# Kernel tuning notes

Measured on AMD Instinct MI355X. Metric: run time of the kernel, lower is better.

## Reference

```python
import jax, jax.numpy as jnp
import numpy as np

NUM_EXPERTS = 8
HIDDEN = 1024
FFN = 2048
TOKENS = 2048


def setup_inputs() -> dict:
    key = jax.random.key(0)
    k_x, k_idx, k_w1, k_w2 = jax.random.split(key, 4)
    scale = 0.02
    x = jax.random.normal(k_x, (TOKENS, HIDDEN), dtype=jnp.float32)
    expert_indices = jax.random.randint(k_idx, (TOKENS,), 0, NUM_EXPERTS, dtype=jnp.int64)
    W1 = jax.random.normal(k_w1, (NUM_EXPERTS, HIDDEN, FFN), dtype=jnp.float32) * scale
    b1 = jnp.zeros((NUM_EXPERTS, FFN), dtype=jnp.float32)
    W2 = jax.random.normal(k_w2, (NUM_EXPERTS, FFN, HIDDEN), dtype=jnp.float32) * scale
    b2 = jnp.zeros((NUM_EXPERTS, HIDDEN), dtype=jnp.float32)
    return {"x": x, "expert_indices": expert_indices, "W1": W1, "b1": b1, "W2": W2, "b2": b2}


def reference(x, expert_indices, W1, b1, W2, b2):
    # Each token routed to one expert's MLP: Linear -> GELU(exact) -> Linear.
    # Dropout is identity in eval mode. Loop is over the small fixed expert set.
    out = jnp.zeros_like(x)
    for e in range(NUM_EXPERTS):
        h = jax.nn.gelu(x @ W1[e] + b1[e], approximate=False)  # [T, FFN]
        y = h @ W2[e] + b2[e]                                   # [T, H]
        mask = (expert_indices == e)[:, None]
        out = out + jnp.where(mask, y, 0.0)
    return out
```

## Files before the change

kernel.cpp:

```cpp
#include <hip/hip_runtime.h>

#define T_TOK 2048
#define HID   1024
#define FFN   2048
#define NEXP  8
#define MAX_SLOTS 40

typedef __attribute__((ext_vector_type(8))) short bf16x8;
typedef __attribute__((ext_vector_type(4))) float f32x4;

__device__ __forceinline__ short f2bf(float f) {
    unsigned u = __builtin_bit_cast(unsigned, f);
    u = (u + 0x7fffu + ((u >> 16) & 1u)) >> 16;
    return (short)u;
}

__device__ __forceinline__ float gelu_exact(float x) {
    return 0.5f * x * (1.0f + erff(x * 0.70710678118654752f));
}

__device__ __forceinline__ void async_cp16(const short* g, short* l) {
    __builtin_amdgcn_global_load_lds(
        (const __attribute__((address_space(1))) unsigned int*)g,
        (__attribute__((address_space(3))) unsigned int*)l, 16, 0, 0);
}

__device__ __forceinline__ void wtrans_body(
        const float* __restrict__ W, short* __restrict__ WT,
        int K, int N, int e, int kblk, int nblk) {
    int tid = threadIdx.x;
    int w = tid >> 6, l = tid & 63;
    int kb = kblk * 32 + w * 8;
    int n4 = nblk * 256 + l * 4;
    const float* src = W + (size_t)e * K * N + (size_t)kb * N + n4;
    float4 v[8];
#pragma unroll
    for (int r = 0; r < 8; r++)
        v[r] = *(const float4*)(src + (size_t)r * N);
    int kpanel = kb >> 6;
    int kc = (kb >> 3) & 7;
    int npanel = n4 >> 7;
    int n_in = n4 & 127;
    int kpanels = K >> 6;
    short* dst = WT + (size_t)e * K * N
               + ((size_t)npanel * kpanels + kpanel) * 8192
               + kc * 1024 + n_in * 8;
#pragma unroll
    for (int j = 0; j < 4; j++) {
        bf16x8 o = {f2bf(((const float*)&v[0])[j]), f2bf(((const float*)&v[1])[j]),
                    f2bf(((const float*)&v[2])[j]), f2bf(((const float*)&v[3])[j]),
                    f2bf(((const float*)&v[4])[j]), f2bf(((const float*)&v[5])[j]),
                    f2bf(((const float*)&v[6])[j]), f2bf(((const float*)&v[7])[j])};
        *(bf16x8*)(dst + j * 8) = o;
    }
}

__global__ __launch_bounds__(256) void prep_kernel(
        const float* __restrict__ x, const int* __restrict__ idx,
        const float* __restrict__ b2,
        const float* __restrict__ W1, const float* __restrict__ W2,
        short* __restrict__ xb, float* __restrict__ out,
        short* __restrict__ W1T, short* __restrict__ W2T,
        int* __restrict__ offs, int* __restrict__ cnts,
        int* __restrict__ tokl,
        int* __restrict__ slot_e, int* __restrict__ slot_t0) {
    int bx = blockIdx.x;
    int tid = threadIdx.x;
    if (bx < 2048) {
        int e = bx >> 8, rem = bx & 255;
        wtrans_body(W1, W1T, HID, FFN, e, rem & 31, rem >> 5);
    } else if (bx < 4096) {
        int b = bx - 2048;
        int e = b >> 8, rem = b & 255;
        wtrans_body(W2, W2T, FFN, HID, e, rem & 63, rem >> 6);
    } else if (bx < 5120) {
        int i = ((bx - 4096) * 256 + tid) * 8;
        float4 v0 = *(const float4*)(x + i);
        float4 v1 = *(const float4*)(x + i + 4);
        bf16x8 r = {f2bf(v0.x), f2bf(v0.y), f2bf(v0.z), f2bf(v0.w),
                    f2bf(v1.x), f2bf(v1.y), f2bf(v1.z), f2bf(v1.w)};
        *(bf16x8*)(xb + i) = r;
    } else if (bx < 7168) {
        int t = bx - 5120;
        int e = idx[t];
        ((float4*)(out + (size_t)t * HID))[tid] =
            ((const float4*)(b2 + (size_t)e * HID))[tid];
    } else {
        __shared__ int c[NEXP], cur[NEXP], o[NEXP];
        if (tid < NEXP) { c[tid] = 0; cur[tid] = 0; }
        __syncthreads();
        for (int t = tid; t < T_TOK; t += 256) atomicAdd(&c[idx[t]], 1);
        __syncthreads();
        if (tid == 0) {
            int s = 0;
            for (int e = 0; e < NEXP; e++) { o[e] = s; s += c[e]; }
            int ns = 0;
            for (int e = 0; e < NEXP; e++)
                for (int t0 = 0; t0 < c[e]; t0 += 64) {
                    slot_e[ns] = e; slot_t0[ns] = t0; ns++;
                }
            for (; ns < MAX_SLOTS; ns++) slot_e[ns] = -1;
        }
        __syncthreads();
        if (tid < NEXP) { offs[tid] = o[tid]; cnts[tid] = c[tid]; }
        for (int t = tid; t < T_TOK; t += 256) {
            int e = idx[t];
            int p = o[e] + atomicAdd(&cur[e], 1);
            tokl[p] = t;
        }
    }
}

__global__ __launch_bounds__(256) void gemm1_kernel(
        const short* __restrict__ xb, const short* __restrict__ W1T,
        const float* __restrict__ b1,
        const int* __restrict__ offs, const int* __restrict__ cnts,
        const int* __restrict__ tokl,
        const int* __restrict__ slot_e, const int* __restrict__ slot_t0,
        short* __restrict__ hg) {
    int s = blockIdx.y;
    int e = slot_e[s];
    if (e < 0) return;
    int t0 = slot_t0[s], count = cnts[e], off = offs[e];
    int n0 = blockIdx.x * 128;

    __shared__ short As[64 * 64];
    __shared__ short Bs[8 * 128 * 8];
    __shared__ int stok[64];

    int tid = threadIdx.x;
    if (tid < 64) {
        int p = t0 + tid;
        stok[tid] = tokl[off + (p < count ? p : count - 1)];
    }
    __syncthreads();

    int w = tid >> 6, l = tid & 63, l15 = l & 15, quad = l >> 4;
    int wm = (w >> 1) * 32, wn = (w & 1) * 64;

    int m0 = w * 16 + (l >> 3), m1 = m0 + 8;
    int cs = l & 7;
    int c0 = (cs - m0) & 7, c1 = (cs - m1) & 7;
    const short* gA0 = xb + (size_t)stok[m0] * HID + c0 * 8;
    const short* gA1 = xb + (size_t)stok[m1] * HID + c1 * 8;
    short* lA0 = As + w * 1024 + l * 8;
    short* lA1 = lA0 + 512;

    const short* Bpan = W1T + (size_t)e * (FFN * HID)
                      + (size_t)(n0 >> 7) * ((HID >> 6) * 8192);
    int bo0 = (2 * w) * 1024 + l * 8;
    int bo1 = bo0 + 1024;
    int bo2 = bo0 + 512;
    int bo3 = bo1 + 512;

    f32x4 acc[2][4];
#pragma unroll
    for (int i = 0; i < 2; i++)
#pragma unroll
        for (int j = 0; j < 4; j++) acc[i][j] = (f32x4){0.f, 0.f, 0.f, 0.f};

    for (int kt = 0; kt < HID / 64; kt++) {
        const short* bp = Bpan + kt * 8192;
        async_cp16(gA0, lA0);
        async_cp16(gA1, lA1);
        async_cp16(bp + bo0, Bs + bo0);
        async_cp16(bp + bo1, Bs + bo1);
        async_cp16(bp + bo2, Bs + bo2);
        async_cp16(bp + bo3, Bs + bo3);
        gA0 += 64; gA1 += 64;
        __syncthreads();
        bf16x8 a[2][2], b[2][4];
#pragma unroll
        for (int kk = 0; kk < 2; kk++) {
#pragma unroll
            for (int mt = 0; mt < 2; mt++) {
                int m = wm + mt * 16 + l15;
                a[kk][mt] = *(const bf16x8*)&As[m * 64 + (((kk * 4 + quad) + m) & 7) * 8];
            }
#pragma unroll
            for (int nt = 0; nt < 4; nt++) {
                int n = wn + nt * 16 + l15;
                b[kk][nt] = *(const bf16x8*)&Bs[(kk * 4 + quad) * 1024 + n * 8];
            }
        }
#pragma unroll
        for (int kk = 0; kk < 2; kk++)
#pragma unroll
            for (int mt = 0; mt < 2; mt++)
#pragma unroll
                for (int nt = 0; nt < 4; nt++)
                    acc[mt][nt] = __builtin_amdgcn_mfma_f32_16x16x32_bf16(
                        a[kk][mt], b[kk][nt], acc[mt][nt], 0, 0, 0);
        __syncthreads();
    }

    const float* b1e = b1 + e * FFN + n0;
#pragma unroll
    for (int mt = 0; mt < 2; mt++) {
        int rbase = wm + mt * 16 + quad * 4;
#pragma unroll
        for (int nt = 0; nt < 4; nt++) {
            int coln = wn + nt * 16 + l15;
            float bb = b1e[coln];
#pragma unroll
            for (int r = 0; r < 4; r++) {
                int p = t0 + rbase + r;
                if (p < count)
                    hg[(size_t)(off + p) * FFN + n0 + coln] =
                        f2bf(gelu_exact(acc[mt][nt][r] + bb));
            }
        }
    }
}

__global__ __launch_bounds__(256) void gemm2_kernel(
        const short* __restrict__ hg, const short* __restrict__ W2T,
        const int* __restrict__ offs, const int* __restrict__ cnts,
        const int* __restrict__ tokl,
        const int* __restrict__ slot_e, const int* __restrict__ slot_t0,
        float* __restrict__ out) {
    int s = blockIdx.y;
    int e = slot_e[s];
    if (e < 0) return;
    int t0 = slot_t0[s], count = cnts[e], off = offs[e];
    int ks = blockIdx.z;
    int n0 = blockIdx.x * 128;

    __shared__ short As[64 * 64];
    __shared__ short Bs[8 * 128 * 8];

    int tid = threadIdx.x;
    int w = tid >> 6, l = tid & 63, l15 = l & 15, quad = l >> 4;
    int wm = (w >> 1) * 32, wn = (w & 1) * 64;

    int m0 = w * 16 + (l >> 3), m1 = m0 + 8;
    int cs = l & 7;
    int c0 = (cs - m0) & 7, c1 = (cs - m1) & 7;
    int g0 = off + (t0 + m0 < count ? t0 + m0 : count - 1);
    int g1 = off + (t0 + m1 < count ? t0 + m1 : count - 1);
    const short* gA0 = hg + (size_t)g0 * FFN + ks * 1024 + c0 * 8;
    const short* gA1 = hg + (size_t)g1 * FFN + ks * 1024 + c1 * 8;
    short* lA0 = As + w * 1024 + l * 8;
    short* lA1 = lA0 + 512;

    const short* Bpan = W2T + (size_t)e * (FFN * HID)
                      + (size_t)(n0 >> 7) * ((FFN >> 6) * 8192)
                      + (size_t)ks * 16 * 8192;
    int bo0 = (2 * w) * 1024 + l * 8;
    int bo1 = bo0 + 1024;
    int bo2 = bo0 + 512;
    int bo3 = bo1 + 512;

    f32x4 acc[2][4];
#pragma unroll
    for (int i = 0; i < 2; i++)
#pragma unroll
        for (int j = 0; j < 4; j++) acc[i][j] = (f32x4){0.f, 0.f, 0.f, 0.f};

    for (int kt = 0; kt < 16; kt++) {
        const short* bp = Bpan + kt * 8192;
        async_cp16(gA0, lA0);
        async_cp16(gA1, lA1);
        async_cp16(bp + bo0, Bs + bo0);
        async_cp16(bp + bo1, Bs + bo1);
        async_cp16(bp + bo2, Bs + bo2);
        async_cp16(bp + bo3, Bs + bo3);
        gA0 += 64; gA1 += 64;
        __syncthreads();
        bf16x8 a[2][2], b[2][4];
#pragma unroll
        for (int kk = 0; kk < 2; kk++) {
#pragma unroll
            for (int mt = 0; mt < 2; mt++) {
                int m = wm + mt * 16 + l15;
                a[kk][mt] = *(const bf16x8*)&As[m * 64 + (((kk * 4 + quad) + m) & 7) * 8];
            }
#pragma unroll
            for (int nt = 0; nt < 4; nt++) {
                int n = wn + nt * 16 + l15;
                b[kk][nt] = *(const bf16x8*)&Bs[(kk * 4 + quad) * 1024 + n * 8];
            }
        }
#pragma unroll
        for (int kk = 0; kk < 2; kk++)
#pragma unroll
            for (int mt = 0; mt < 2; mt++)
#pragma unroll
                for (int nt = 0; nt < 4; nt++)
                    acc[mt][nt] = __builtin_amdgcn_mfma_f32_16x16x32_bf16(
                        a[kk][mt], b[kk][nt], acc[mt][nt], 0, 0, 0);
        __syncthreads();
    }

#pragma unroll
    for (int mt = 0; mt < 2; mt++) {
        int rbase = wm + mt * 16 + quad * 4;
#pragma unroll
        for (int nt = 0; nt < 4; nt++) {
            int coln = n0 + wn + nt * 16 + l15;
#pragma unroll
            for (int r = 0; r < 4; r++) {
                int p = t0 + rbase + r;
                if (p < count) {
                    int tok = tokl[off + p];
                    atomicAdd(out + (size_t)tok * HID + coln, acc[mt][nt][r]);
                }
            }
        }
    }
}

extern "C" void kernel_launch(void* const* d_in, const int* in_sizes, int n_in,
                              void* d_out, int out_size, void* d_ws, size_t ws_size,
                              hipStream_t stream) {
    const float* x   = (const float*)d_in[0];
    const int*   idx = (const int*)d_in[1];
    const float* W1  = (const float*)d_in[2];
    const float* b1  = (const float*)d_in[3];
    const float* W2  = (const float*)d_in[4];
    const float* b2  = (const float*)d_in[5];
    float* out = (float*)d_out;

    const size_t META = 32768;
    int*   offs    = (int*)d_ws;
    int*   cnts    = offs + 8;
    int*   tokl    = offs + 16;
    int*   slot_e  = offs + 16 + T_TOK;
    int*   slot_t0 = slot_e + MAX_SLOTS;
    char*  base    = (char*)d_ws + META;
    short* xb  = (short*)base;
    short* hg  = (short*)(base + (size_t)T_TOK * HID * 2);
    short* W1T = (short*)(base + (size_t)T_TOK * HID * 2 + (size_t)T_TOK * FFN * 2);
    short* W2T = W1T + (size_t)NEXP * FFN * HID;

    prep_kernel<<<7169, 256, 0, stream>>>(
        x, idx, b2, W1, W2, xb, out, W1T, W2T,
        offs, cnts, tokl, slot_e, slot_t0);

    gemm1_kernel<<<dim3(FFN / 128, MAX_SLOTS), 256, 0, stream>>>(
        xb, W1T, b1, offs, cnts, tokl, slot_e, slot_t0, hg);
    gemm2_kernel<<<dim3(HID / 128, MAX_SLOTS, 2), 256, 0, stream>>>(
        hg, W2T, offs, cnts, tokl, slot_e, slot_t0, out);
}
```

Baseline: 224.6 us.

## Enlarge GEMM M-tile to 128, double-buffer LDS, and swizzle weight panels

Both expert GEMMs move from 64x128 to 128x128 block tiles with 4x4 MFMA accumulators per wave, and routing slots now cover 128 tokens, with MAX_SLOTS cut to 32. The K loop uses two LDS buffers: the async global-to-LDS copy for the next K tile is issued right after the barrier, so it overlaps the MFMAs on the current tile. The weight pre-transpose writes an n-major, XOR-style swizzled panel layout matching the new B-fragment reads, and each prep block now converts two K-chunks. The aim is more reuse per loaded tile, hidden load latency and fewer prep blocks. The cost is higher register and LDS use per block, which may lower occupancy, and more padded rows for experts whose token counts do not fill a 128-row tile.

```diff
diff --git a/kernel.cpp b/kernel.cpp
--- a/kernel.cpp
+++ b/kernel.cpp
@@ -4,7 +4,7 @@
 #define HID   1024
 #define FFN   2048
 #define NEXP  8
-#define MAX_SLOTS 40
+#define MAX_SLOTS 32
 
 typedef __attribute__((ext_vector_type(8))) short bf16x8;
 typedef __attribute__((ext_vector_type(4))) float f32x4;
@@ -27,31 +27,30 @@
 
 __device__ __forceinline__ void wtrans_body(
         const float* __restrict__ W, short* __restrict__ WT,
-        int K, int N, int e, int kblk, int nblk) {
+        int K, int N, int e, int kpanel, int npair) {
     int tid = threadIdx.x;
     int w = tid >> 6, l = tid & 63;
-    int kb = kblk * 32 + w * 8;
-    int n4 = nblk * 256 + l * 4;
-    const float* src = W + (size_t)e * K * N + (size_t)kb * N + n4;
-    float4 v[8];
-#pragma unroll
-    for (int r = 0; r < 8; r++)
-        v[r] = *(const float4*)(src + (size_t)r * N);
-    int kpanel = kb >> 6;
-    int kc = (kb >> 3) & 7;
-    int npanel = n4 >> 7;
-    int n_in = n4 & 127;
-    int kpanels = K >> 6;
-    short* dst = WT + (size_t)e * K * N
-               + ((size_t)npanel * kpanels + kpanel) * 8192
-               + kc * 1024 + n_in * 8;
-#pragma unroll
-    for (int j = 0; j < 4; j++) {
-        bf16x8 o = {f2bf(((const float*)&v[0])[j]), f2bf(((const float*)&v[1])[j]),
-                    f2bf(((const float*)&v[2])[j]), f2bf(((const float*)&v[3])[j]),
-                    f2bf(((const float*)&v[4])[j]), f2bf(((const float*)&v[5])[j]),
-                    f2bf(((const float*)&v[6])[j]), f2bf(((const float*)&v[7])[j])};
-        *(bf16x8*)(dst + j * 8) = o;
+    int n4 = npair * 256 + l * 4;
+    int npanel = n4 >> 7, n_in = n4 & 127;
+    short* dstp = WT + (size_t)e * K * N
+                + ((size_t)npanel * (K >> 6) + kpanel) * 8192;
+    const float* We = W + (size_t)e * K * N;
+#pragma unroll
+    for (int h = 0; h < 2; h++) {
+        int kc = w + h * 4;
+        const float* src = We + (size_t)(kpanel * 64 + kc * 8) * N + n4;
+        float4 v[8];
+#pragma unroll
+        for (int r = 0; r < 8; r++) v[r] = *(const float4*)(src + (size_t)r * N);
+#pragma unroll
+        for (int j = 0; j < 4; j++) {
+            bf16x8 o = {f2bf(((const float*)&v[0])[j]), f2bf(((const float*)&v[1])[j]),
+                        f2bf(((const float*)&v[2])[j]), f2bf(((const float*)&v[3])[j]),
+                        f2bf(((const float*)&v[4])[j]), f2bf(((const float*)&v[5])[j]),
+                        f2bf(((const float*)&v[6])[j]), f2bf(((const float*)&v[7])[j])};
+            int n = n_in + j;
+            *(bf16x8*)(dstp + n * 64 + ((kc + n) & 7) * 8) = o;
+        }
     }
 }
 
@@ -66,22 +65,22 @@
         int* __restrict__ slot_e, int* __restrict__ slot_t0) {
     int bx = blockIdx.x;
     int tid = threadIdx.x;
-    if (bx < 2048) {
-        int e = bx >> 8, rem = bx & 255;
-        wtrans_body(W1, W1T, HID, FFN, e, rem & 31, rem >> 5);
-    } else if (bx < 4096) {
-        int b = bx - 2048;
-        int e = b >> 8, rem = b & 255;
-        wtrans_body(W2, W2T, FFN, HID, e, rem & 63, rem >> 6);
-    } else if (bx < 5120) {
-        int i = ((bx - 4096) * 256 + tid) * 8;
+    if (bx < 1024) {
+        int e = bx >> 7, rem = bx & 127;
+        wtrans_body(W1, W1T, HID, FFN, e, rem >> 3, rem & 7);
+    } else if (bx < 2048) {
+        int b = bx - 1024;
+        int e = b >> 7, rem = b & 127;
+        wtrans_body(W2, W2T, FFN, HID, e, rem >> 2, rem & 3);
+    } else if (bx < 3072) {
+        int i = ((bx - 2048) * 256 + tid) * 8;
         float4 v0 = *(const float4*)(x + i);
         float4 v1 = *(const float4*)(x + i + 4);
         bf16x8 r = {f2bf(v0.x), f2bf(v0.y), f2bf(v0.z), f2bf(v0.w),
                     f2bf(v1.x), f2bf(v1.y), f2bf(v1.z), f2bf(v1.w)};
         *(bf16x8*)(xb + i) = r;
-    } else if (bx < 7168) {
-        int t = bx - 5120;
+    } else if (bx < 5120) {
+        int t = bx - 3072;
         int e = idx[t];
         ((float4*)(out + (size_t)t * HID))[tid] =
             ((const float4*)(b2 + (size_t)e * HID))[tid];
@@ -96,7 +95,7 @@
             for (int e = 0; e < NEXP; e++) { o[e] = s; s += c[e]; }
             int ns = 0;
             for (int e = 0; e < NEXP; e++)
-                for (int t0 = 0; t0 < c[e]; t0 += 64) {
+                for (int t0 = 0; t0 < c[e]; t0 += 128) {
                     slot_e[ns] = e; slot_t0[ns] = t0; ns++;
                 }
             for (; ns < MAX_SLOTS; ns++) slot_e[ns] = -1;
@@ -124,79 +123,74 @@
     int t0 = slot_t0[s], count = cnts[e], off = offs[e];
     int n0 = blockIdx.x * 128;
 
-    __shared__ short As[64 * 64];
-    __shared__ short Bs[8 * 128 * 8];
-    __shared__ int stok[64];
+    __shared__ short As[2][128 * 64];
+    __shared__ short Bs[2][128 * 64];
 
     int tid = threadIdx.x;
-    if (tid < 64) {
-        int p = t0 + tid;
-        stok[tid] = tokl[off + (p < count ? p : count - 1)];
-    }
-    __syncthreads();
-
     int w = tid >> 6, l = tid & 63, l15 = l & 15, quad = l >> 4;
-    int wm = (w >> 1) * 32, wn = (w & 1) * 64;
-
-    int m0 = w * 16 + (l >> 3), m1 = m0 + 8;
-    int cs = l & 7;
-    int c0 = (cs - m0) & 7, c1 = (cs - m1) & 7;
-    const short* gA0 = xb + (size_t)stok[m0] * HID + c0 * 8;
-    const short* gA1 = xb + (size_t)stok[m1] * HID + c1 * 8;
-    short* lA0 = As + w * 1024 + l * 8;
-    short* lA1 = lA0 + 512;
+    int wm = (w >> 1) * 64, wn = (w & 1) * 64;
+
+    const short* srcA[4];
+    int arow[4];
+#pragma unroll
+    for (int i = 0; i < 4; i++) {
+        int row = w * 32 + i * 8 + (l >> 3);
+        arow[i] = row;
+        int c = ((l & 7) - row) & 7;
+        int p = t0 + row;
+        int g = tokl[off + (p < count ? p : count - 1)];
+        srcA[i] = xb + (size_t)g * HID + c * 8;
+    }
+    int sbase = w * 2048 + l * 8;
 
     const short* Bpan = W1T + (size_t)e * (FFN * HID)
                       + (size_t)(n0 >> 7) * ((HID >> 6) * 8192);
-    int bo0 = (2 * w) * 1024 + l * 8;
-    int bo1 = bo0 + 1024;
-    int bo2 = bo0 + 512;
-    int bo3 = bo1 + 512;
-
-    f32x4 acc[2][4];
-#pragma unroll
-    for (int i = 0; i < 2; i++)
+
+    f32x4 acc[4][4];
+#pragma unroll
+    for (int i = 0; i < 4; i++)
 #pragma unroll
         for (int j = 0; j < 4; j++) acc[i][j] = (f32x4){0.f, 0.f, 0.f, 0.f};
 
-    for (int kt = 0; kt < HID / 64; kt++) {
-        const short* bp = Bpan + kt * 8192;
-        async_cp16(gA0, lA0);
-        async_cp16(gA1, lA1);
-        async_cp16(bp + bo0, Bs + bo0);
-        async_cp16(bp + bo1, Bs + bo1);
-        async_cp16(bp + bo2, Bs + bo2);
-        async_cp16(bp + bo3, Bs + bo3);
-        gA0 += 64; gA1 += 64;
-        __syncthreads();
-        bf16x8 a[2][2], b[2][4];
+#define G1_DMA(BUF, KT) {                                                    \
+    _Pragma("unroll") for (int i = 0; i < 4; i++)                            \
+        async_cp16(srcA[i] + (KT) * 64, &As[BUF][sbase + i * 512]);          \
+    const short* bp = Bpan + (size_t)(KT) * 8192;                            \
+    _Pragma("unroll") for (int i = 0; i < 4; i++)                            \
+        async_cp16(bp + sbase + i * 512, &Bs[BUF][sbase + i * 512]); }
+
+    G1_DMA(0, 0);
+    const int NK = HID / 64;
+    for (int kt = 0; kt < NK; kt++) {
+        __syncthreads();
+        int cur = kt & 1;
+        if (kt + 1 < NK) G1_DMA(1 - cur, kt + 1);
 #pragma unroll
         for (int kk = 0; kk < 2; kk++) {
-#pragma unroll
-            for (int mt = 0; mt < 2; mt++) {
+            int cq = kk * 4 + quad;
+            bf16x8 a[4], b[4];
+#pragma unroll
+            for (int mt = 0; mt < 4; mt++) {
                 int m = wm + mt * 16 + l15;
-                a[kk][mt] = *(const bf16x8*)&As[m * 64 + (((kk * 4 + quad) + m) & 7) * 8];
+                a[mt] = *(const bf16x8*)&As[cur][m * 64 + ((cq + m) & 7) * 8];
             }
 #pragma unroll
             for (int nt = 0; nt < 4; nt++) {
                 int n = wn + nt * 16 + l15;
-                b[kk][nt] = *(const bf16x8*)&Bs[(kk * 4 + quad) * 1024 + n * 8];
-            }
-        }
-#pragma unroll
-        for (int kk = 0; kk < 2; kk++)
-#pragma unroll
-            for (int mt = 0; mt < 2; mt++)
+                b[nt] = *(const bf16x8*)&Bs[cur][n * 64 + ((cq + n) & 7) * 8];
+            }
+#pragma unroll
+            for (int mt = 0; mt < 4; mt++)
 #pragma unroll
                 for (int nt = 0; nt < 4; nt++)
                     acc[mt][nt] = __builtin_amdgcn_mfma_f32_16x16x32_bf16(
-                        a[kk][mt], b[kk][nt], acc[mt][nt], 0, 0, 0);
-        __syncthreads();
+                        a[mt], b[nt], acc[mt][nt], 0, 0, 0);
+        }
     }
 
     const float* b1e = b1 + e * FFN + n0;
 #pragma unroll
-    for (int mt = 0; mt < 2; mt++) {
+    for (int mt = 0; mt < 4; mt++) {
         int rbase = wm + mt * 16 + quad * 4;
 #pragma unroll
         for (int nt = 0; nt < 4; nt++) {
@@ -226,74 +220,72 @@
     int ks = blockIdx.z;
     int n0 = blockIdx.x * 128;
 
-    __shared__ short As[64 * 64];
-    __shared__ short Bs[8 * 128 * 8];
+    __shared__ short As[2][128 * 64];
+    __shared__ short Bs[2][128 * 64];
 
     int tid = threadIdx.x;
     int w = tid >> 6, l = tid & 63, l15 = l & 15, quad = l >> 4;
-    int wm = (w >> 1) * 32, wn = (w & 1) * 64;
-
-    int m0 = w * 16 + (l >> 3), m1 = m0 + 8;
-    int cs = l & 7;
-    int c0 = (cs - m0) & 7, c1 = (cs - m1) & 7;
-    int g0 = off + (t0 + m0 < count ? t0 + m0 : count - 1);
-    int g1 = off + (t0 + m1 < count ? t0 + m1 : count - 1);
-    const short* gA0 = hg + (size_t)g0 * FFN + ks * 1024 + c0 * 8;
-    const short* gA1 = hg + (size_t)g1 * FFN + ks * 1024 + c1 * 8;
-    short* lA0 = As + w * 1024 + l * 8;
-    short* lA1 = lA0 + 512;
+    int wm = (w >> 1) * 64, wn = (w & 1) * 64;
+
+    const short* srcA[4];
+#pragma unroll
+    for (int i = 0; i < 4; i++) {
+        int row = w * 32 + i * 8 + (l >> 3);
+        int c = ((l & 7) - row) & 7;
+        int p = t0 + row;
+        int g = off + (p < count ? p : count - 1);
+        srcA[i] = hg + (size_t)g * FFN + ks * 1024 + c * 8;
+    }
+    int sbase = w * 2048 + l * 8;
 
     const short* Bpan = W2T + (size_t)e * (FFN * HID)
                       + (size_t)(n0 >> 7) * ((FFN >> 6) * 8192)
                       + (size_t)ks * 16 * 8192;
-    int bo0 = (2 * w) * 1024 + l * 8;
-    int bo1 = bo0 + 1024;
-    int bo2 = bo0 + 512;
-    int bo3 = bo1 + 512;
-
-    f32x4 acc[2][4];
-#pragma unroll
-    for (int i = 0; i < 2; i++)
+
+    f32x4 acc[4][4];
+#pragma unroll
+    for (int i = 0; i < 4; i++)
 #pragma unroll
         for (int j = 0; j < 4; j++) acc[i][j] = (f32x4){0.f, 0.f, 0.f, 0.f};
 
-    for (int kt = 0; kt < 16; kt++) {
-        const short* bp = Bpan + kt * 8192;
-        async_cp16(gA0, lA0);
-        async_cp16(gA1, lA1);
-        async_cp16(bp + bo0, Bs + bo0);
-        async_cp16(bp + bo1, Bs + bo1);
-        async_cp16(bp + bo2, Bs + bo2);
-        async_cp16(bp + bo3, Bs + bo3);
-        gA0 += 64; gA1 += 64;
-        __syncthreads();
-        bf16x8 a[2][2], b[2][4];
+#define G2_DMA(BUF, KT) {                                                    \
+    _Pragma("unroll") for (int i = 0; i < 4; i++)                            \
+        async_cp16(srcA[i] + (KT) * 64, &As[BUF][sbase + i * 512]);          \
+    const short* bp = Bpan + (size_t)(KT) * 8192;                            \
+    _Pragma("unroll") for (int i = 0; i < 4; i++)                            \
+        async_cp16(bp + sbase + i * 512, &Bs[BUF][sbase + i * 512]); }
+
+    G2_DMA(0, 0);
+    const int NK = 16;
+    for (int kt = 0; kt < NK; kt++) {
+        __syncthreads();
+        int cur = kt & 1;
+        if (kt + 1 < NK) G2_DMA(1 - cur, kt + 1);
 #pragma unroll
         for (int kk = 0; kk < 2; kk++) {
-#pragma unroll
-            for (int mt = 0; mt < 2; mt++) {
+            int cq = kk * 4 + quad;
+            bf16x8 a[4], b[4];
+#pragma unroll
+            for (int mt = 0; mt < 4; mt++) {
                 int m = wm + mt * 16 + l15;
-                a[kk][mt] = *(const bf16x8*)&As[m * 64 + (((kk * 4 + quad) + m) & 7) * 8];
+                a[mt] = *(const bf16x8*)&As[cur][m * 64 + ((cq + m) & 7) * 8];
             }
 #pragma unroll
             for (int nt = 0; nt < 4; nt++) {
                 int n = wn + nt * 16 + l15;
-                b[kk][nt] = *(const bf16x8*)&Bs[(kk * 4 + quad) * 1024 + n * 8];
-            }
-        }
-#pragma unroll
-        for (int kk = 0; kk < 2; kk++)
-#pragma unroll
-            for (int mt = 0; mt < 2; mt++)
+                b[nt] = *(const bf16x8*)&Bs[cur][n * 64 + ((cq + n) & 7) * 8];
+            }
+#pragma unroll
+            for (int mt = 0; mt < 4; mt++)
 #pragma unroll
                 for (int nt = 0; nt < 4; nt++)
                     acc[mt][nt] = __builtin_amdgcn_mfma_f32_16x16x32_bf16(
-                        a[kk][mt], b[kk][nt], acc[mt][nt], 0, 0, 0);
-        __syncthreads();
-    }
-
-#pragma unroll
-    for (int mt = 0; mt < 2; mt++) {
+                        a[mt], b[nt], acc[mt][nt], 0, 0, 0);
+        }
+    }
+
+#pragma unroll
+    for (int mt = 0; mt < 4; mt++) {
         int rbase = wm + mt * 16 + quad * 4;
 #pragma unroll
         for (int nt = 0; nt < 4; nt++) {
@@ -333,7 +325,7 @@
     short* W1T = (short*)(base + (size_t)T_TOK * HID * 2 + (size_t)T_TOK * FFN * 2);
     short* W2T = W1T + (size_t)NEXP * FFN * HID;
 
-    prep_kernel<<<7169, 256, 0, stream>>>(
+    prep_kernel<<<5121, 256, 0, stream>>>(
         x, idx, b2, W1, W2, xb, out, W1T, W2T,
         offs, cnts, tokl, slot_e, slot_t0);
 
```

New measurement: 272.7 us. +21.4%, slower.
